# Performance work log

Hardware: AMD Instinct MI355X
Metric: run time of the kernel (lower is better)

The kernel has to match this reference:

```python
import jax, jax.numpy as jnp
import numpy as np

N_NODES = 100000
N_EDGES = 1000000
NUM_FEATURES = 64
HIDDEN = 64
NUM_GRAPHS = 128


def setup_inputs() -> dict:
    key = jax.random.key(0)
    ks = jax.random.split(key, 12)
    x = jax.random.normal(ks[0], (N_NODES, NUM_FEATURES), dtype=jnp.float32)
    edge_index = jax.random.randint(ks[1], (2, N_EDGES), 0, N_NODES, dtype=jnp.int64)
    edge_weight = jax.random.uniform(ks[2], (N_EDGES,), dtype=jnp.float32)
    batch = jnp.sort(jax.random.randint(ks[3], (N_NODES,), 0, NUM_GRAPHS, dtype=jnp.int64))
    s1 = 1.0 / np.sqrt(NUM_FEATURES)
    s2 = 1.0 / np.sqrt(HIDDEN)
    # GraphConv layer 1: lin_rel (with bias) applied to aggregated msgs, lin_root (no bias)
    w1_rel = jax.random.uniform(ks[4], (HIDDEN, NUM_FEATURES), jnp.float32, -s1, s1)
    b1_rel = jax.random.uniform(ks[5], (HIDDEN,), jnp.float32, -s1, s1)
    w1_root = jax.random.uniform(ks[6], (HIDDEN, NUM_FEATURES), jnp.float32, -s1, s1)
    # GraphConv layer 2
    w2_rel = jax.random.uniform(ks[7], (HIDDEN, HIDDEN), jnp.float32, -s2, s2)
    b2_rel = jax.random.uniform(ks[8], (HIDDEN,), jnp.float32, -s2, s2)
    w2_root = jax.random.uniform(ks[9], (HIDDEN, HIDDEN), jnp.float32, -s2, s2)
    # final Linear(hidden, 1)
    w_lin = jax.random.uniform(ks[10], (1, HIDDEN), jnp.float32, -s2, s2)
    b_lin = jax.random.uniform(ks[11], (1,), jnp.float32, -s2, s2)
    return {
        "x": x, "edge_index": edge_index, "edge_weight": edge_weight, "batch": batch,
        "w1_rel": w1_rel, "b1_rel": b1_rel, "w1_root": w1_root,
        "w2_rel": w2_rel, "b2_rel": b2_rel, "w2_root": w2_root,
        "w_lin": w_lin, "b_lin": b_lin,
    }


def graph_conv(x, edge_index, edge_weight, w_rel, b_rel, w_root):
    # messages: x[src] * e, scatter-add into dst  (gather-scale-scatter)
    src, dst = edge_index[0], edge_index[1]
    msgs = x[src] * edge_weight[:, None]                      # [E, F]
    aggr = jax.ops.segment_sum(msgs, dst, num_segments=x.shape[0])  # [N, F]
    return aggr @ w_rel.T + b_rel + x @ w_root.T


def reference(x, edge_index, edge_weight, batch,
              w1_rel, b1_rel, w1_root, w2_rel, b2_rel, w2_root, w_lin, b_lin):
    h = graph_conv(x, edge_index, edge_weight, w1_rel, b1_rel, w1_root)
    h = jax.nn.relu(h)
    h = graph_conv(h, edge_index, edge_weight, w2_rel, b2_rel, w2_root)
    # global_mean_pool over graph ids
    sums = jax.ops.segment_sum(h, batch, num_segments=NUM_GRAPHS)          # [G, H]
    counts = jax.ops.segment_sum(jnp.ones((h.shape[0],), h.dtype), batch,
                                 num_segments=NUM_GRAPHS)                  # [G]
    pooled = sums / jnp.maximum(counts, 1.0)[:, None]
    # dropout(p=0.5) in eval mode is identity
    return pooled @ w_lin.T + b_lin                                        # [G, 1]
```

## Files before the change

kernel.cpp:

```cpp
#include <hip/hip_runtime.h>
#include <hip/hip_bf16.h>


#define N_NODES 100000
#define N_EDGES 1000000
#define NGRAPHS 128
#define BN 512
#define NBUCK ((N_NODES + BN - 1) / BN)
#define FILL_T 16
#define FILL_TILE (256 * FILL_T)
#define FILL_NB ((N_EDGES + FILL_TILE - 1) / FILL_TILE)

typedef __attribute__((ext_vector_type(8))) short bf16x8;
typedef __attribute__((ext_vector_type(8))) unsigned short u16x8;
typedef __attribute__((ext_vector_type(4))) float f32x4;

__device__ __forceinline__ unsigned short f2bf(float f) {
    unsigned u = __float_as_uint(f);
    unsigned r = (u + 0x7FFFu + ((u >> 16) & 1u)) >> 16;
    return (unsigned short)r;
}
__device__ __forceinline__ float bf2f(unsigned short h) {
    return __uint_as_float(((unsigned)h) << 16);
}

__global__ __launch_bounds__(256) void prep_kernel(
    const float* __restrict__ w1rel, const float* __restrict__ w1root,
    const float* __restrict__ w2rel, const float* __restrict__ w2root,
    const float* __restrict__ wlin, const float* __restrict__ b2rel,
    const float* __restrict__ blin, unsigned short* __restrict__ whirel,
    unsigned short* __restrict__ wlorel, unsigned short* __restrict__ whiroot,
    unsigned short* __restrict__ wloroot, float* __restrict__ u,
    float* __restrict__ v, float* __restrict__ C) {
    int tid = threadIdx.x;
    for (int i = tid; i < 4096; i += 256) {
        float a = w1rel[i];
        unsigned short hi = f2bf(a);
        whirel[i] = hi;
        wlorel[i] = f2bf(a - bf2f(hi));
        float b = w1root[i];
        unsigned short hb = f2bf(b);
        whiroot[i] = hb;
        wloroot[i] = f2bf(b - bf2f(hb));
    }
    if (tid < 64) {
        float uu = 0.f, vv = 0.f;
        for (int h = 0; h < 64; ++h) {
            float wl = wlin[h];
            uu += wl * w2rel[h * 64 + tid];
            vv += wl * w2root[h * 64 + tid];
        }
        u[tid] = uu;
        v[tid] = vv;
    }
    if (tid == 0) {
        float c = blin[0];
        for (int h = 0; h < 64; ++h) c += wlin[h] * b2rel[h];
        *C = c;
    }
}

__global__ __launch_bounds__(256) void cvt_x_kernel(
    const float* __restrict__ x, unsigned short* __restrict__ xh, int n8) {
    int i = blockIdx.x * 256 + threadIdx.x;
    if (i >= n8) return;
    const float4* xp = (const float4*)x + (size_t)i * 2;
    float4 a = xp[0], b = xp[1];
    u16x8 o;
    o[0] = f2bf(a.x); o[1] = f2bf(a.y); o[2] = f2bf(a.z); o[3] = f2bf(a.w);
    o[4] = f2bf(b.x); o[5] = f2bf(b.y); o[6] = f2bf(b.z); o[7] = f2bf(b.w);
    *((u16x8*)xh + i) = o;
}

__global__ __launch_bounds__(256) void bucket_hist(const int* __restrict__ ei,
                                                   int* __restrict__ bcount,
                                                   int E) {
    __shared__ int lh[NBUCK];
    int tid = threadIdx.x;
    for (int i = tid; i < NBUCK; i += 256) lh[i] = 0;
    __syncthreads();
    for (int e = blockIdx.x * 256 + tid; e < E; e += gridDim.x * 256)
        atomicAdd(&lh[ei[E + e] >> 9], 1);
    __syncthreads();
    for (int i = tid; i < NBUCK; i += 256) {
        int c = lh[i];
        if (c) atomicAdd(&bcount[i], c);
    }
}

__global__ void bucket_scan(const int* __restrict__ bcount,
                            int* __restrict__ boff, int* __restrict__ cursor) {
    __shared__ int s[256];
    int t = threadIdx.x;
    int v = (t < NBUCK) ? bcount[t] : 0;
    s[t] = v;
    __syncthreads();
    for (int off = 1; off < 256; off <<= 1) {
        int x = (t >= off) ? s[t - off] : 0;
        __syncthreads();
        s[t] += x;
        __syncthreads();
    }
    if (t < NBUCK) {
        boff[t] = s[t] - v;
        cursor[t] = s[t] - v;
    }
    if (t == 255) boff[NBUCK] = s[255];
}

__global__ __launch_bounds__(256) void bucket_fill(
    const int* __restrict__ ei, const float* __restrict__ ew,
    int* __restrict__ cursor, int2* __restrict__ ebuf, int E) {
    __shared__ int lh[NBUCK];
    __shared__ int gbase[NBUCK];
    int tid = threadIdx.x;
    for (int i = tid; i < NBUCK; i += 256) lh[i] = 0;
    __syncthreads();
    int base = blockIdx.x * FILL_TILE;
    int2 rec[FILL_T];
    int meta[FILL_T];
#pragma unroll
    for (int i = 0; i < FILL_T; ++i) {
        int e = base + i * 256 + tid;
        meta[i] = -1;
        if (e < E) {
            int src = ei[e];
            int dst = ei[E + e];
            int b = dst >> 9;
            int r = atomicAdd(&lh[b], 1);
            rec[i].x = src | ((dst & (BN - 1)) << 17);
            rec[i].y = __float_as_int(ew[e]);
            meta[i] = (b << 13) | r;
        }
    }
    __syncthreads();
    for (int i = tid; i < NBUCK; i += 256) {
        int c = lh[i];
        gbase[i] = c ? atomicAdd(&cursor[i], c) : 0;
    }
    __syncthreads();
#pragma unroll
    for (int i = 0; i < FILL_T; ++i) {
        if (meta[i] >= 0) {
            int b = meta[i] >> 13;
            int r = meta[i] & 8191;
            ebuf[gbase[b] + r] = rec[i];
        }
    }
}

__global__ __launch_bounds__(512) void csr_build(
    const int* __restrict__ boff, const int2* __restrict__ ebuf,
    const int* __restrict__ batch, int* __restrict__ row_ptr,
    int2* __restrict__ csr, int N) {
    __shared__ int s[BN];
    int b = blockIdx.x;
    int t = threadIdx.x;
    int beg = boff[b], end = boff[b + 1];
    s[t] = 0;
    __syncthreads();
    for (int j = beg + t; j < end; j += 512)
        atomicAdd(&s[(ebuf[j].x >> 17) & (BN - 1)], 1);
    __syncthreads();
    int v = s[t];
    for (int off = 1; off < BN; off <<= 1) {
        int x = (t >= off) ? s[t - off] : 0;
        __syncthreads();
        s[t] += x;
        __syncthreads();
    }
    int excl = s[t] - v;
    int gidx = b * BN + t;
    if (gidx <= N) row_ptr[gidx] = beg + excl;
    __syncthreads();
    s[t] = excl;
    __syncthreads();
    for (int j = beg + t; j < end; j += 512) {
        int2 rec = ebuf[j];
        int dlo = (rec.x >> 17) & (BN - 1);
        int g = batch[b * BN + dlo];
        int r = atomicAdd(&s[dlo], 1);
        int2 o;
        o.x = (rec.x & 0x1FFFF) | (g << 17);
        o.y = rec.y;
        csr[beg + r] = o;
    }
}

__global__ __launch_bounds__(256) void gather_kernel(
    const unsigned short* __restrict__ xh, const int* __restrict__ row_ptr,
    const int2* __restrict__ csr, unsigned short* __restrict__ aggr, int N,
    int chunk) {
    int lane = threadIdx.x & 63;
    int wid = (blockIdx.x * blockDim.x + threadIdx.x) >> 6;
    int g = lane >> 4;
    int c = lane & 15;
    int n0 = wid * chunk;
    int n1 = min(n0 + chunk, N);
    for (int node = n0; node < n1; ++node) {
        int beg = row_ptr[node], end = row_ptr[node + 1];
        float4 acc = {0.f, 0.f, 0.f, 0.f};
        for (int j0 = beg; j0 < end; j0 += 64) {
            int cnt = min(64, end - j0);
            int2 e = {0, 0};
            if (lane < cnt) e = csr[j0 + lane];
            for (int k = 0; k < cnt; k += 4) {
                int myk = k + g;
                int sj = __shfl(e.x, myk) & 0x1FFFF;
                float wj = __int_as_float(__shfl(e.y, myk));
                if (myk < cnt) {
                    ushort4 xv =
                        *(const ushort4*)(xh + (size_t)sj * 64 + c * 4);
                    acc.x += wj * bf2f(xv.x);
                    acc.y += wj * bf2f(xv.y);
                    acc.z += wj * bf2f(xv.z);
                    acc.w += wj * bf2f(xv.w);
                }
            }
        }
#pragma unroll
        for (int off = 16; off < 64; off <<= 1) {
            acc.x += __shfl_xor(acc.x, off);
            acc.y += __shfl_xor(acc.y, off);
            acc.z += __shfl_xor(acc.z, off);
            acc.w += __shfl_xor(acc.w, off);
        }
        if (lane < 16) {
            ushort4 o;
            o.x = f2bf(acc.x);
            o.y = f2bf(acc.y);
            o.z = f2bf(acc.z);
            o.w = f2bf(acc.w);
            *(ushort4*)(aggr + (size_t)node * 64 + c * 4) = o;
        }
    }
}

__global__ __launch_bounds__(256, 2) void dense_kernel(
    const unsigned short* __restrict__ aggr,
    const unsigned short* __restrict__ xh,
    const unsigned short* __restrict__ whirel,
    const unsigned short* __restrict__ wlorel,
    const unsigned short* __restrict__ whiroot,
    const unsigned short* __restrict__ wloroot,
    const float* __restrict__ b1rel, const float* __restrict__ u,
    const float* __restrict__ v, float* __restrict__ p, float* __restrict__ q,
    int N) {
    int lane = threadIdx.x & 63;
    int wave = (blockIdx.x << 2) + (threadIdx.x >> 6);
    int nb = wave * 16;
    if (nb >= N) return;
    int lo4 = lane & 15;
    int quad = lane >> 4;

    f32x4 acc[4];
#pragma unroll
    for (int t = 0; t < 4; ++t) acc[t] = (f32x4){0.f, 0.f, 0.f, 0.f};

    for (int s = 0; s < 2; ++s) {
        bf16x8 Aa = *(const bf16x8*)(aggr + (size_t)(nb + lo4) * 64 + s * 32 +
                                     quad * 8);
        bf16x8 Ax = *(const bf16x8*)(xh + (size_t)(nb + lo4) * 64 + s * 32 +
                                     quad * 8);
#pragma unroll
        for (int t = 0; t < 4; ++t) {
            int off = (t * 16 + lo4) * 64 + s * 32 + quad * 8;
            bf16x8 bhr = *(const bf16x8*)(whirel + off);
            bf16x8 blr = *(const bf16x8*)(wlorel + off);
            bf16x8 bhx = *(const bf16x8*)(whiroot + off);
            bf16x8 blx = *(const bf16x8*)(wloroot + off);
            acc[t] = __builtin_amdgcn_mfma_f32_16x16x32_bf16(Aa, bhr, acc[t],
                                                             0, 0, 0);
            acc[t] = __builtin_amdgcn_mfma_f32_16x16x32_bf16(Aa, blr, acc[t],
                                                             0, 0, 0);
            acc[t] = __builtin_amdgcn_mfma_f32_16x16x32_bf16(Ax, bhx, acc[t],
                                                             0, 0, 0);
            acc[t] = __builtin_amdgcn_mfma_f32_16x16x32_bf16(Ax, blx, acc[t],
                                                             0, 0, 0);
        }
    }

    float pc[4] = {0.f, 0.f, 0.f, 0.f};
    float qc[4] = {0.f, 0.f, 0.f, 0.f};
#pragma unroll
    for (int t = 0; t < 4; ++t) {
        float bb = b1rel[t * 16 + lo4];
        float uu = u[t * 16 + lo4];
        float vv = v[t * 16 + lo4];
#pragma unroll
        for (int r = 0; r < 4; ++r) {
            float h1 = fmaxf(acc[t][r] + bb, 0.f);
            pc[r] += uu * h1;
            qc[r] += vv * h1;
        }
    }
#pragma unroll
    for (int off = 1; off < 16; off <<= 1) {
#pragma unroll
        for (int r = 0; r < 4; ++r) {
            pc[r] += __shfl_xor(pc[r], off);
            qc[r] += __shfl_xor(qc[r], off);
        }
    }
    if (lo4 == 0) {
        f32x4 po = {pc[0], pc[1], pc[2], pc[3]};
        f32x4 qo = {qc[0], qc[1], qc[2], qc[3]};
        *(f32x4*)(p + nb + quad * 4) = po;
        *(f32x4*)(q + nb + quad * 4) = qo;
    }
}

#define PT_EPT 4
#define PT_EPW (64 * PT_EPT)
__global__ __launch_bounds__(256) void pool_t_flat(
    const int2* __restrict__ csr, const float* __restrict__ p,
    float* __restrict__ gp, int E) {
    __shared__ float lgp[NGRAPHS];
    int tid = threadIdx.x;
    if (tid < NGRAPHS) lgp[tid] = 0.f;
    __syncthreads();
    int lane = tid & 63;
    int wid = (blockIdx.x * 256 + tid) >> 6;
    int base = wid * PT_EPW;
    float acc = 0.f;
    int curg = -1;
#pragma unroll
    for (int i = 0; i < PT_EPT; ++i) {
        int j = base + i * 64 + lane;
        if (j < E) {
            int2 e = csr[j];
            int g = ((unsigned)e.x) >> 17;
            float val = __int_as_float(e.y) * p[e.x & 0x1FFFF];
            if (g != curg) {
                if (curg >= 0) atomicAdd(&lgp[curg], acc);
                curg = g;
                acc = 0.f;
            }
            acc += val;
        }
    }
    if (curg >= 0) atomicAdd(&lgp[curg], acc);
    __syncthreads();
    if (tid < NGRAPHS) {
        float t = lgp[tid];
        if (t != 0.f) atomicAdd(&gp[tid], t);
    }
}

__global__ __launch_bounds__(256) void pool_s(const float* __restrict__ q,
                                              const int* __restrict__ batch,
                                              float* __restrict__ gq,
                                              float* __restrict__ gc, int N) {
    __shared__ float lgq[NGRAPHS], lgc[NGRAPHS];
    int tid = threadIdx.x;
    if (tid < NGRAPHS) {
        lgq[tid] = 0.f;
        lgc[tid] = 0.f;
    }
    __syncthreads();
    for (int i = blockIdx.x * 256 + tid; i < N; i += gridDim.x * 256) {
        int g = batch[i];
        atomicAdd(&lgq[g], q[i]);
        atomicAdd(&lgc[g], 1.f);
    }
    __syncthreads();
    if (tid < NGRAPHS) {
        if (lgc[tid] != 0.f) {
            atomicAdd(&gq[tid], lgq[tid]);
            atomicAdd(&gc[tid], lgc[tid]);
        }
    }
}

__global__ void final_kernel(const float* __restrict__ gp,
                             const float* __restrict__ gq,
                             const float* __restrict__ gc,
                             const float* __restrict__ C,
                             float* __restrict__ out) {
    int g = threadIdx.x;
    float c = fmaxf(gc[g], 1.0f);
    out[g] = (gp[g] + gq[g]) / c + *C;
}

extern "C" void kernel_launch(void* const* d_in, const int* in_sizes, int n_in,
                              void* d_out, int out_size, void* d_ws,
                              size_t ws_size, hipStream_t stream) {
    const float* x      = (const float*)d_in[0];
    const int*   ei     = (const int*)d_in[1];
    const float* ew     = (const float*)d_in[2];
    const int*   batch  = (const int*)d_in[3];
    const float* w1rel  = (const float*)d_in[4];
    const float* b1rel  = (const float*)d_in[5];
    const float* w1root = (const float*)d_in[6];
    const float* w2rel  = (const float*)d_in[7];
    const float* b2rel  = (const float*)d_in[8];
    const float* w2root = (const float*)d_in[9];
    const float* wlin   = (const float*)d_in[10];
    const float* blin   = (const float*)d_in[11];
    float* out = (float*)d_out;

    char* wsb = (char*)d_ws;
    int2* csr  = (int2*)wsb;
    unsigned short* aggr = (unsigned short*)(wsb + (size_t)N_EDGES * 8);
    int2* ebuf = (int2*)aggr;
    char* tail = wsb + (size_t)N_EDGES * 8 + (size_t)N_NODES * 128;
    unsigned short* whirel  = (unsigned short*)tail;
    unsigned short* wlorel  = whirel + 4096;
    unsigned short* whiroot = wlorel + 4096;
    unsigned short* wloroot = whiroot + 4096;
    float* p  = (float*)(wloroot + 4096);
    float* q  = p + N_NODES;
    float* u  = q + N_NODES;
    float* v  = u + 64;
    float* C  = v + 64;
    int*   bcount = (int*)(C + 1);
    float* gp = (float*)(bcount + NBUCK);
    float* gq = gp + NGRAPHS;
    float* gc = gq + NGRAPHS;
    int*   boff   = (int*)(gc + NGRAPHS);
    int*   cursor = boff + (NBUCK + 1);
    int*   row_ptr = cursor + NBUCK;
    unsigned short* xh = (unsigned short*)(row_ptr + N_NODES + 2);

    hipMemsetAsync(bcount, 0, (NBUCK + 3 * NGRAPHS) * sizeof(int), stream);

    prep_kernel<<<1, 256, 0, stream>>>(w1rel, w1root, w2rel, w2root, wlin,
                                       b2rel, blin, whirel, wlorel, whiroot,
                                       wloroot, u, v, C);
    cvt_x_kernel<<<(N_NODES * 64 / 8 + 255) / 256, 256, 0, stream>>>(
        x, xh, N_NODES * 64 / 8);

    bucket_hist<<<256, 256, 0, stream>>>(ei, bcount, N_EDGES);
    bucket_scan<<<1, 256, 0, stream>>>(bcount, boff, cursor);
    bucket_fill<<<FILL_NB, 256, 0, stream>>>(ei, ew, cursor, ebuf, N_EDGES);
    csr_build<<<NBUCK, 512, 0, stream>>>(boff, ebuf, batch, row_ptr, csr,
                                         N_NODES);

    {
        int blocks = 2048;
        int waves = blocks * 4;
        int chunk = (N_NODES + waves - 1) / waves;
        gather_kernel<<<blocks, 256, 0, stream>>>(xh, row_ptr, csr, aggr,
                                                  N_NODES, chunk);
    }
    {
        int tiles = N_NODES / 16;
        int blocks = (tiles + 3) / 4;
        dense_kernel<<<blocks, 256, 0, stream>>>(aggr, xh, whirel, wlorel,
                                                 whiroot, wloroot, b1rel, u, v,
                                                 p, q, N_NODES);
    }
    {
        int blocks = (N_EDGES + 4 * PT_EPW - 1) / (4 * PT_EPW);
        pool_t_flat<<<blocks, 256, 0, stream>>>(csr, p, gp, N_EDGES);
    }
    pool_s<<<196, 256, 0, stream>>>(q, batch, gq, gc, N_NODES);
    final_kernel<<<1, NGRAPHS, 0, stream>>>(gp, gq, gc, C, out);
}
```

Measured before the change: 234.1 us.

## Fuse gather with dense MFMA via LDS, merge prep/cvt and pool kernels

The edge gather is fused into the dense MFMA kernel. Each wave aggregates 16 nodes into a padded LDS tile and then feeds it straight to the MFMAs, so the bf16 aggr buffer no longer makes a round trip through global memory. The weight-prep and x-conversion kernels are merged into one launch, and the two pooling kernels are merged into one grid split by block index, which cuts launch count. The cost is that each wave now walks its 16 nodes serially before any MFMA work, and the gather's grid changes from 2048 persistent blocks to one wave per 16-node tile, which may hurt load balance and latency hiding.

```diff
diff --git a/kernel.cpp b/kernel.cpp
--- a/kernel.cpp
+++ b/kernel.cpp
@@ -10,6 +10,8 @@
 #define FILL_T 16
 #define FILL_TILE (256 * FILL_T)
 #define FILL_NB ((N_EDGES + FILL_TILE - 1) / FILL_TILE)
+#define NTILES (N_NODES / 16)
+#define AST 72
 
 typedef __attribute__((ext_vector_type(8))) short bf16x8;
 typedef __attribute__((ext_vector_type(8))) unsigned short u16x8;
@@ -24,7 +26,8 @@
     return __uint_as_float(((unsigned)h) << 16);
 }
 
-__global__ __launch_bounds__(256) void prep_kernel(
+__global__ __launch_bounds__(256) void prep_cvt_kernel(
+    const float* __restrict__ x, unsigned short* __restrict__ xh, int n8,
     const float* __restrict__ w1rel, const float* __restrict__ w1root,
     const float* __restrict__ w2rel, const float* __restrict__ w2root,
     const float* __restrict__ wlin, const float* __restrict__ b2rel,
@@ -33,15 +36,25 @@
     unsigned short* __restrict__ wloroot, float* __restrict__ u,
     float* __restrict__ v, float* __restrict__ C) {
     int tid = threadIdx.x;
-    for (int i = tid; i < 4096; i += 256) {
-        float a = w1rel[i];
+    int i = blockIdx.x * 256 + tid;
+    if (i < n8) {
+        const float4* xp = (const float4*)x + (size_t)i * 2;
+        float4 a = xp[0], b = xp[1];
+        u16x8 o;
+        o[0] = f2bf(a.x); o[1] = f2bf(a.y); o[2] = f2bf(a.z); o[3] = f2bf(a.w);
+        o[4] = f2bf(b.x); o[5] = f2bf(b.y); o[6] = f2bf(b.z); o[7] = f2bf(b.w);
+        *((u16x8*)xh + i) = o;
+        return;
+    }
+    for (int k = tid; k < 4096; k += 256) {
+        float a = w1rel[k];
         unsigned short hi = f2bf(a);
-        whirel[i] = hi;
-        wlorel[i] = f2bf(a - bf2f(hi));
-        float b = w1root[i];
+        whirel[k] = hi;
+        wlorel[k] = f2bf(a - bf2f(hi));
+        float b = w1root[k];
         unsigned short hb = f2bf(b);
-        whiroot[i] = hb;
-        wloroot[i] = f2bf(b - bf2f(hb));
+        whiroot[k] = hb;
+        wloroot[k] = f2bf(b - bf2f(hb));
     }
     if (tid < 64) {
         float uu = 0.f, vv = 0.f;
@@ -58,18 +71,6 @@
         for (int h = 0; h < 64; ++h) c += wlin[h] * b2rel[h];
         *C = c;
     }
-}
-
-__global__ __launch_bounds__(256) void cvt_x_kernel(
-    const float* __restrict__ x, unsigned short* __restrict__ xh, int n8) {
-    int i = blockIdx.x * 256 + threadIdx.x;
-    if (i >= n8) return;
-    const float4* xp = (const float4*)x + (size_t)i * 2;
-    float4 a = xp[0], b = xp[1];
-    u16x8 o;
-    o[0] = f2bf(a.x); o[1] = f2bf(a.y); o[2] = f2bf(a.z); o[3] = f2bf(a.w);
-    o[4] = f2bf(b.x); o[5] = f2bf(b.y); o[6] = f2bf(b.z); o[7] = f2bf(b.w);
-    *((u16x8*)xh + i) = o;
 }
 
 __global__ __launch_bounds__(256) void bucket_hist(const int* __restrict__ ei,
@@ -187,17 +188,27 @@
     }
 }
 
-__global__ __launch_bounds__(256) void gather_kernel(
+__global__ __launch_bounds__(256) void gather_dense_kernel(
     const unsigned short* __restrict__ xh, const int* __restrict__ row_ptr,
-    const int2* __restrict__ csr, unsigned short* __restrict__ aggr, int N,
-    int chunk) {
+    const int2* __restrict__ csr, const unsigned short* __restrict__ whirel,
+    const unsigned short* __restrict__ wlorel,
+    const unsigned short* __restrict__ whiroot,
+    const unsigned short* __restrict__ wloroot,
+    const float* __restrict__ b1rel, const float* __restrict__ u,
+    const float* __restrict__ v, float* __restrict__ p, float* __restrict__ q,
+    int ntiles) {
+    __shared__ unsigned short arow[4][16 * AST];
     int lane = threadIdx.x & 63;
-    int wid = (blockIdx.x * blockDim.x + threadIdx.x) >> 6;
+    int wv = threadIdx.x >> 6;
+    int wave = (blockIdx.x << 2) + wv;
+    if (wave >= ntiles) return;
+    unsigned short* my = &arow[wv][0];
+    int nb = wave * 16;
     int g = lane >> 4;
     int c = lane & 15;
-    int n0 = wid * chunk;
-    int n1 = min(n0 + chunk, N);
-    for (int node = n0; node < n1; ++node) {
+
+    for (int nl = 0; nl < 16; ++nl) {
+        int node = nb + nl;
         int beg = row_ptr[node], end = row_ptr[node + 1];
         float4 acc = {0.f, 0.f, 0.f, 0.f};
         for (int j0 = beg; j0 < end; j0 += 64) {
@@ -231,35 +242,18 @@
             o.y = f2bf(acc.y);
             o.z = f2bf(acc.z);
             o.w = f2bf(acc.w);
-            *(ushort4*)(aggr + (size_t)node * 64 + c * 4) = o;
-        }
-    }
-}
-
-__global__ __launch_bounds__(256, 2) void dense_kernel(
-    const unsigned short* __restrict__ aggr,
-    const unsigned short* __restrict__ xh,
-    const unsigned short* __restrict__ whirel,
-    const unsigned short* __restrict__ wlorel,
-    const unsigned short* __restrict__ whiroot,
-    const unsigned short* __restrict__ wloroot,
-    const float* __restrict__ b1rel, const float* __restrict__ u,
-    const float* __restrict__ v, float* __restrict__ p, float* __restrict__ q,
-    int N) {
-    int lane = threadIdx.x & 63;
-    int wave = (blockIdx.x << 2) + (threadIdx.x >> 6);
-    int nb = wave * 16;
-    if (nb >= N) return;
+            *(ushort4*)(my + nl * AST + c * 4) = o;
+        }
+    }
+
     int lo4 = lane & 15;
     int quad = lane >> 4;
-
-    f32x4 acc[4];
-#pragma unroll
-    for (int t = 0; t < 4; ++t) acc[t] = (f32x4){0.f, 0.f, 0.f, 0.f};
-
+    f32x4 acc4[4];
+#pragma unroll
+    for (int t = 0; t < 4; ++t) acc4[t] = (f32x4){0.f, 0.f, 0.f, 0.f};
+#pragma unroll
     for (int s = 0; s < 2; ++s) {
-        bf16x8 Aa = *(const bf16x8*)(aggr + (size_t)(nb + lo4) * 64 + s * 32 +
-                                     quad * 8);
+        bf16x8 Aa = *(const bf16x8*)(my + lo4 * AST + s * 32 + quad * 8);
         bf16x8 Ax = *(const bf16x8*)(xh + (size_t)(nb + lo4) * 64 + s * 32 +
                                      quad * 8);
 #pragma unroll
@@ -269,14 +263,14 @@
             bf16x8 blr = *(const bf16x8*)(wlorel + off);
             bf16x8 bhx = *(const bf16x8*)(whiroot + off);
             bf16x8 blx = *(const bf16x8*)(wloroot + off);
-            acc[t] = __builtin_amdgcn_mfma_f32_16x16x32_bf16(Aa, bhr, acc[t],
-                                                             0, 0, 0);
-            acc[t] = __builtin_amdgcn_mfma_f32_16x16x32_bf16(Aa, blr, acc[t],
-                                                             0, 0, 0);
-            acc[t] = __builtin_amdgcn_mfma_f32_16x16x32_bf16(Ax, bhx, acc[t],
-                                                             0, 0, 0);
-            acc[t] = __builtin_amdgcn_mfma_f32_16x16x32_bf16(Ax, blx, acc[t],
-                                                             0, 0, 0);
+            acc4[t] = __builtin_amdgcn_mfma_f32_16x16x32_bf16(Aa, bhr, acc4[t],
+                                                              0, 0, 0);
+            acc4[t] = __builtin_amdgcn_mfma_f32_16x16x32_bf16(Aa, blr, acc4[t],
+                                                              0, 0, 0);
+            acc4[t] = __builtin_amdgcn_mfma_f32_16x16x32_bf16(Ax, bhx, acc4[t],
+                                                              0, 0, 0);
+            acc4[t] = __builtin_amdgcn_mfma_f32_16x16x32_bf16(Ax, blx, acc4[t],
+                                                              0, 0, 0);
         }
     }
 
@@ -289,7 +283,7 @@
         float vv = v[t * 16 + lo4];
 #pragma unroll
         for (int r = 0; r < 4; ++r) {
-            float h1 = fmaxf(acc[t][r] + bb, 0.f);
+            float h1 = fmaxf(acc4[t][r] + bb, 0.f);
             pc[r] += uu * h1;
             qc[r] += vv * h1;
         }
@@ -312,62 +306,57 @@
 
 #define PT_EPT 4
 #define PT_EPW (64 * PT_EPT)
-__global__ __launch_bounds__(256) void pool_t_flat(
+#define PT_NB ((N_EDGES + 4 * PT_EPW - 1) / (4 * PT_EPW))
+#define PS_NB 98
+__global__ __launch_bounds__(256) void pool_both(
     const int2* __restrict__ csr, const float* __restrict__ p,
-    float* __restrict__ gp, int E) {
-    __shared__ float lgp[NGRAPHS];
+    const float* __restrict__ q, const int* __restrict__ batch,
+    float* __restrict__ gp, float* __restrict__ gq, float* __restrict__ gc,
+    int E, int N) {
+    __shared__ float lbuf[2 * NGRAPHS];
     int tid = threadIdx.x;
-    if (tid < NGRAPHS) lgp[tid] = 0.f;
-    __syncthreads();
-    int lane = tid & 63;
-    int wid = (blockIdx.x * 256 + tid) >> 6;
-    int base = wid * PT_EPW;
-    float acc = 0.f;
-    int curg = -1;
-#pragma unroll
-    for (int i = 0; i < PT_EPT; ++i) {
-        int j = base + i * 64 + lane;
-        if (j < E) {
-            int2 e = csr[j];
-            int g = ((unsigned)e.x) >> 17;
-            float val = __int_as_float(e.y) * p[e.x & 0x1FFFF];
-            if (g != curg) {
-                if (curg >= 0) atomicAdd(&lgp[curg], acc);
-                curg = g;
-                acc = 0.f;
+    lbuf[tid] = 0.f;
+    __syncthreads();
+    if (blockIdx.x < PT_NB) {
+        int lane = tid & 63;
+        int wid = (blockIdx.x * 256 + tid) >> 6;
+        int base = wid * PT_EPW;
+        float acc = 0.f;
+        int curg = -1;
+#pragma unroll
+        for (int i = 0; i < PT_EPT; ++i) {
+            int j = base + i * 64 + lane;
+            if (j < E) {
+                int2 e = csr[j];
+                int g = ((unsigned)e.x) >> 17;
+                float val = __int_as_float(e.y) * p[e.x & 0x1FFFF];
+                if (g != curg) {
+                    if (curg >= 0) atomicAdd(&lbuf[curg], acc);
+                    curg = g;
+                    acc = 0.f;
+                }
+                acc += val;
             }
-            acc += val;
-        }
-    }
-    if (curg >= 0) atomicAdd(&lgp[curg], acc);
-    __syncthreads();
-    if (tid < NGRAPHS) {
-        float t = lgp[tid];
-        if (t != 0.f) atomicAdd(&gp[tid], t);
-    }
-}
-
-__global__ __launch_bounds__(256) void pool_s(const float* __restrict__ q,
-                                              const int* __restrict__ batch,
-                                              float* __restrict__ gq,
-                                              float* __restrict__ gc, int N) {
-    __shared__ float lgq[NGRAPHS], lgc[NGRAPHS];
-    int tid = threadIdx.x;
-    if (tid < NGRAPHS) {
-        lgq[tid] = 0.f;
-        lgc[tid] = 0.f;
-    }
-    __syncthreads();
-    for (int i = blockIdx.x * 256 + tid; i < N; i += gridDim.x * 256) {
-        int g = batch[i];
-        atomicAdd(&lgq[g], q[i]);
-        atomicAdd(&lgc[g], 1.f);
-    }
-    __syncthreads();
-    if (tid < NGRAPHS) {
-        if (lgc[tid] != 0.f) {
-            atomicAdd(&gq[tid], lgq[tid]);
-            atomicAdd(&gc[tid], lgc[tid]);
+        }
+        if (curg >= 0) atomicAdd(&lbuf[curg], acc);
+        __syncthreads();
+        if (tid < NGRAPHS) {
+            float t = lbuf[tid];
+            if (t != 0.f) atomicAdd(&gp[tid], t);
+        }
+    } else {
+        int bid = blockIdx.x - PT_NB;
+        for (int i = bid * 256 + tid; i < N; i += PS_NB * 256) {
+            int g = batch[i];
+            atomicAdd(&lbuf[g], q[i]);
+            atomicAdd(&lbuf[NGRAPHS + g], 1.f);
+        }
+        __syncthreads();
+        if (tid < NGRAPHS) {
+            if (lbuf[NGRAPHS + tid] != 0.f) {
+                atomicAdd(&gq[tid], lbuf[tid]);
+                atomicAdd(&gc[tid], lbuf[NGRAPHS + tid]);
+            }
         }
     }
 }
@@ -401,9 +390,8 @@
 
     char* wsb = (char*)d_ws;
     int2* csr  = (int2*)wsb;
-    unsigned short* aggr = (unsigned short*)(wsb + (size_t)N_EDGES * 8);
-    int2* ebuf = (int2*)aggr;
-    char* tail = wsb + (size_t)N_EDGES * 8 + (size_t)N_NODES * 128;
+    int2* ebuf = (int2*)(wsb + (size_t)N_EDGES * 8);
+    char* tail = wsb + (size_t)N_EDGES * 16;
     unsigned short* whirel  = (unsigned short*)tail;
     unsigned short* wlorel  = whirel + 4096;
     unsigned short* whiroot = wlorel + 4096;
@@ -424,11 +412,10 @@
 
     hipMemsetAsync(bcount, 0, (NBUCK + 3 * NGRAPHS) * sizeof(int), stream);
 
-    prep_kernel<<<1, 256, 0, stream>>>(w1rel, w1root, w2rel, w2root, wlin,
-                                       b2rel, blin, whirel, wlorel, whiroot,
-                                       wloroot, u, v, C);
-    cvt_x_kernel<<<(N_NODES * 64 / 8 + 255) / 256, 256, 0, stream>>>(
-        x, xh, N_NODES * 64 / 8);
+    int n8 = N_NODES * 64 / 8;
+    prep_cvt_kernel<<<n8 / 256 + 1, 256, 0, stream>>>(
+        x, xh, n8, w1rel, w1root, w2rel, w2root, wlin, b2rel, blin, whirel,
+        wlorel, whiroot, wloroot, u, v, C);
 
     bucket_hist<<<256, 256, 0, stream>>>(ei, bcount, N_EDGES);
     bucket_scan<<<1, 256, 0, stream>>>(bcount, boff, cursor);
@@ -436,24 +423,11 @@
     csr_build<<<NBUCK, 512, 0, stream>>>(boff, ebuf, batch, row_ptr, csr,
                                          N_NODES);
 
-    {
-        int blocks = 2048;
-        int waves = blocks * 4;
-        int chunk = (N_NODES + waves - 1) / waves;
-        gather_kernel<<<blocks, 256, 0, stream>>>(xh, row_ptr, csr, aggr,
-                                                  N_NODES, chunk);
-    }
-    {
-        int tiles = N_NODES / 16;
-        int blocks = (tiles + 3) / 4;
-        dense_kernel<<<blocks, 256, 0, stream>>>(aggr, xh, whirel, wlorel,
-                                                 whiroot, wloroot, b1rel, u, v,
-                                                 p, q, N_NODES);
-    }
-    {
-        int blocks = (N_EDGES + 4 * PT_EPW - 1) / (4 * PT_EPW);
-        pool_t_flat<<<blocks, 256, 0, stream>>>(csr, p, gp, N_EDGES);
-    }
-    pool_s<<<196, 256, 0, stream>>>(q, batch, gq, gc, N_NODES);
+    gather_dense_kernel<<<(NTILES + 3) / 4, 256, 0, stream>>>(
+        xh, row_ptr, csr, whirel, wlorel, whiroot, wloroot, b1rel, u, v, p, q,
+        NTILES);
+
+    pool_both<<<PT_NB + PS_NB, 256, 0, stream>>>(csr, p, q, batch, gp, gq, gc,
+                                                 N_EDGES, N_NODES);
     final_kernel<<<1, NGRAPHS, 0, stream>>>(gp, gq, gc, C, out);
 }
```

After: 223.1 us. -4.7%, faster.
